# Performance work log

Hardware: AMD Instinct MI355X
Metric: run time of the kernel (lower is better)

The kernel has to match this reference:

```python
import jax, jax.numpy as jnp
import numpy as np
import math

ALPHA = 2.0  # spikingjelly surrogate.ATan default alpha
NB_STEPS, NUM_IN, NUM_HID, NUM_OUT = 100, 784, 100, 10
BATCH = 1024
TAU_LIF = 2.0

@jax.custom_vjp
def atan_spike(x):
    # Heaviside forward, ATan surrogate backward
    return (x >= 0.0).astype(x.dtype)

def _atan_fwd(x):
    return atan_spike(x), x

def _atan_bwd(x, g):
    return (g * (ALPHA / 2.0) / (1.0 + (jnp.pi / 2.0 * ALPHA * x) ** 2),)

atan_spike.defvjp(_atan_fwd, _atan_bwd)


def setup_inputs() -> dict:
    key = jax.random.key(0)
    ks = jax.random.split(key, 3)
    x = jax.random.normal(ks[0], (BATCH, NB_STEPS, NUM_IN), jnp.float32)
    tau_syn = 2.0
    # spikingjelly SynapseFilter(learnable=True): w init = -log(tau - 1)
    w_syn1 = jnp.asarray(-math.log(tau_syn - 1.0), jnp.float32)
    w_syn2 = jnp.asarray(-math.log(tau_syn - 1.0), jnp.float32)
    W1 = jax.random.normal(ks[1], (NUM_HID, NUM_IN), jnp.float32) / np.sqrt(NUM_IN).astype(np.float32)
    b1 = jnp.zeros((NUM_HID,), jnp.float32)
    W2 = jax.random.normal(ks[2], (NUM_OUT, NUM_HID), jnp.float32) / np.sqrt(NUM_HID).astype(np.float32)
    b2 = jnp.zeros((NUM_OUT,), jnp.float32)
    return dict(x=x, w_syn1=w_syn1, W1=W1, b1=b1, w_syn2=w_syn2, W2=W2, b2=b2)


def reference(x, w_syn1, W1, b1, w_syn2, W2, b2):
    B = x.shape[0]
    inv1 = jax.nn.sigmoid(w_syn1)  # 1/tau of filter 1
    inv2 = jax.nn.sigmoid(w_syn2)
    s1 = jnp.zeros((B, NUM_IN), x.dtype)
    v1 = jnp.zeros((B, NUM_HID), x.dtype)
    s2 = jnp.zeros((B, NUM_HID), x.dtype)
    v2 = jnp.zeros((B, NUM_OUT), x.dtype)

    def step(carry, xt):
        s1, v1, s2, v2 = carry
        # SynapseFilter 1: s = s - s*sigmoid(w) + in
        s1 = s1 - s1 * inv1 + xt
        h1 = s1 @ W1.T + b1
        # LIF 1: decay_input=True, v_reset=0: v += (x - (v - 0)) / tau
        v1 = v1 + (h1 - v1) / TAU_LIF
        sp1 = atan_spike(v1 - 1.0)       # v_threshold = 1.0
        v1 = v1 * (1.0 - sp1)            # hard reset to v_reset = 0
        # SynapseFilter 2
        s2 = s2 - s2 * inv2 + sp1
        h2 = s2 @ W2.T + b2
        # LIF 2: v_reset=None (soft reset), v_threshold=0, decay_input=True
        v2 = v2 + (h2 - v2) / TAU_LIF
        sp2 = atan_spike(v2 - 0.0)
        v2 = v2 - sp2 * 0.0              # soft reset subtracts spike*threshold (=0)
        return (s1, v1, s2, v2), None

    (s1, v1, s2, v2), _ = jax.lax.scan(step, (s1, v1, s2, v2), jnp.swapaxes(x, 0, 1))
    # Net.forward returns self.fc[-1].v: final membrane potential of last LIF
    return v2
```

## Files before the change

### kernel.cpp

```cpp
#include <hip/hip_runtime.h>
#include <math.h>


#define NSTEPS 100
#define NHID 100
#define KDIM 784
#define BK 16
#define NOUT 10

__global__ __launch_bounds__(256, 4)
void snn_fused(const float* __restrict__ X, const float* __restrict__ wsyn1p,
               const float* __restrict__ W1, const float* __restrict__ b1,
               const float* __restrict__ wsyn2p, const float* __restrict__ W2,
               const float* __restrict__ b2, float* __restrict__ out) {
  __shared__ float Xs[BK][130];
  __shared__ float Ws[BK][104];
  __shared__ float Cs[25][104];
  __shared__ float zsh[NHID];

  const int tid = threadIdx.x;
  const int l   = tid & 63;
  const int wu  = __builtin_amdgcn_readfirstlane(tid >> 6);
  const int cbase = 28 * wu;
  const long b  = blockIdx.x;
  const float* __restrict__ Xb = X + b * (NSTEPS * KDIM);

  float acc0[28], acc1[28];
#pragma unroll
  for (int c = 0; c < 28; ++c) { acc0[c] = 0.f; acc1[c] = 0.f; }

  const int sr  = tid >> 2;
  const int skq = tid & 3;

  for (int kt = 0; kt < KDIM; kt += BK) {
    const float4 va = *(const float4*)(Xb + sr * KDIM + kt + 4 * skq);
    const int t1 = (sr + 64 < NSTEPS) ? (sr + 64) : (NSTEPS - 1);
    const float4 vb = *(const float4*)(Xb + t1 * KDIM + kt + 4 * skq);
    {
      float2 p0 = {va.x, vb.x}, p1 = {va.y, vb.y};
      float2 p2 = {va.z, vb.z}, p3 = {va.w, vb.w};
      *(float2*)&Xs[4 * skq + 0][2 * sr] = p0;
      *(float2*)&Xs[4 * skq + 1][2 * sr] = p1;
      *(float2*)&Xs[4 * skq + 2][2 * sr] = p2;
      *(float2*)&Xs[4 * skq + 3][2 * sr] = p3;
    }
    for (int i = tid; i < 4 * NHID; i += 256) {
      const int j = i >> 2, kq = i & 3;
      const float4 v = *(const float4*)(W1 + (size_t)j * KDIM + kt + 4 * kq);
      Ws[4 * kq + 0][j] = v.x;
      Ws[4 * kq + 1][j] = v.y;
      Ws[4 * kq + 2][j] = v.z;
      Ws[4 * kq + 3][j] = v.w;
    }
    __syncthreads();

#pragma unroll
    for (int k = 0; k < BK; ++k) {
      const float2 xp = *(const float2*)&Xs[k][2 * l];
#pragma unroll
      for (int c4 = 0; c4 < 7; ++c4) {
        const float4 wv = *(const float4*)&Ws[k][cbase + 4 * c4];
        acc0[4*c4+0] = fmaf(xp.x, wv.x, acc0[4*c4+0]);
        acc0[4*c4+1] = fmaf(xp.x, wv.y, acc0[4*c4+1]);
        acc0[4*c4+2] = fmaf(xp.x, wv.z, acc0[4*c4+2]);
        acc0[4*c4+3] = fmaf(xp.x, wv.w, acc0[4*c4+3]);
        acc1[4*c4+0] = fmaf(xp.y, wv.x, acc1[4*c4+0]);
        acc1[4*c4+1] = fmaf(xp.y, wv.y, acc1[4*c4+1]);
        acc1[4*c4+2] = fmaf(xp.y, wv.z, acc1[4*c4+2]);
        acc1[4*c4+3] = fmaf(xp.y, wv.w, acc1[4*c4+3]);
      }
    }
    __syncthreads();
  }

  const float inv1 = 1.f / (1.f + expf(-wsyn1p[0]));
  const float inv2 = 1.f / (1.f + expf(-wsyn2p[0]));
  const float bj = (tid < NHID) ? b1[tid] : 0.f;
  const int ncols = (cbase + 28 <= NHID) ? 28 : (NHID - cbase);
  float S = 0.f, v1 = 0.f, s2 = 0.f, z = 0.f;
  float at = 0x1p-100f;

  for (int q = 0; q < 4; ++q) {
    const int r0 = l - 25 * q;
    const int r1 = l + 64 - 25 * q;
    if (r0 >= 0 && r0 < 25) {
      for (int c = 0; c < ncols; ++c) Cs[r0][cbase + c] = acc0[c];
    }
    if (r1 >= 0 && r1 < 25) {
      for (int c = 0; c < ncols; ++c) Cs[r1][cbase + c] = acc1[c];
    }
    __syncthreads();
    if (tid < NHID) {
#pragma unroll
      for (int tt = 0; tt < 25; ++tt) {
        const float u = Cs[tt][tid];
        S = S - S * inv1 + u;
        const float h = S + bj;
        v1 = v1 + (h - v1) * 0.5f;
        const float sp = (v1 >= 1.0f) ? 1.0f : 0.0f;
        v1 = v1 * (1.0f - sp);
        s2 = s2 - s2 * inv2 + sp;
        z  = fmaf(at, s2, z);
        at *= 2.0f;
      }
    }
    __syncthreads();
  }

  if (tid < NHID) zsh[tid] = z;
  __syncthreads();

  if (tid < NOUT) {
    float a = b2[tid];
    const float* __restrict__ wrow = W2 + tid * NHID;
#pragma unroll
    for (int jj = 0; jj < NHID; ++jj) a = fmaf(zsh[jj], wrow[jj], a);
    out[b * NOUT + tid] = a;
  }
}

extern "C" void kernel_launch(void* const* d_in, const int* in_sizes, int n_in,
                              void* d_out, int out_size, void* d_ws, size_t ws_size,
                              hipStream_t stream) {
  const float* x     = (const float*)d_in[0];
  const float* wsyn1 = (const float*)d_in[1];
  const float* W1    = (const float*)d_in[2];
  const float* b1    = (const float*)d_in[3];
  const float* wsyn2 = (const float*)d_in[4];
  const float* W2    = (const float*)d_in[5];
  const float* b2    = (const float*)d_in[6];
  float* out = (float*)d_out;

  snn_fused<<<dim3(1024), dim3(256), 0, stream>>>(x, wsyn1, W1, b1, wsyn2, W2,
                                                  b2, out);
}
```

Baseline: 642.3 us.

## Process two batch rows per block with 4x25 register tiles and prefetching

Each block now handles two batch elements (512 blocks), giving each thread a 4-row by 25-column accumulator tile so every W1 tile loaded into shared memory is reused across twice as many rows. It also adds register prefetch of the next X/W1 tile to overlap global loads with FMAs, and removes one barrier per k-step. This cuts redundant W1 traffic and raises FMA-to-LDS-load ratio, at the cost of more registers (launch bounds lowered to 2 blocks/SM) and fewer blocks for latency hiding.

Result: faster. 561.7 us (-12.5%).

```diff
diff --git a/kernel.cpp b/kernel.cpp
--- a/kernel.cpp
+++ b/kernel.cpp
@@ -8,92 +8,126 @@
 #define BK 16
 #define NOUT 10
 
-__global__ __launch_bounds__(256, 4)
-void snn_fused(const float* __restrict__ X, const float* __restrict__ wsyn1p,
-               const float* __restrict__ W1, const float* __restrict__ b1,
-               const float* __restrict__ wsyn2p, const float* __restrict__ W2,
-               const float* __restrict__ b2, float* __restrict__ out) {
-  __shared__ float Xs[BK][130];
-  __shared__ float Ws[BK][104];
-  __shared__ float Cs[25][104];
-  __shared__ float zsh[NHID];
+__global__ __launch_bounds__(256, 2)
+void snn_fused2(const float* __restrict__ X, const float* __restrict__ wsyn1p,
+                const float* __restrict__ W1, const float* __restrict__ b1,
+                const float* __restrict__ wsyn2p, const float* __restrict__ W2,
+                const float* __restrict__ b2, float* __restrict__ out) {
+  __shared__ float Xs[BK][256];
+  __shared__ float Ws[BK][112];
+  __shared__ float Cs[2][25][106];
+  __shared__ float zsh[2][NHID];
 
   const int tid = threadIdx.x;
   const int l   = tid & 63;
-  const int wu  = __builtin_amdgcn_readfirstlane(tid >> 6);
-  const int cbase = 28 * wu;
-  const long b  = blockIdx.x;
-  const float* __restrict__ Xb = X + b * (NSTEPS * KDIM);
+  const int cg  = __builtin_amdgcn_readfirstlane(tid >> 6);
+  const long b0 = 2L * blockIdx.x;
 
-  float acc0[28], acc1[28];
+  const int sb = tid >> 7;
+  const int st = ((tid & 127) < NSTEPS) ? (tid & 127) : (NSTEPS - 1);
+  const float* __restrict__ Xrow = X + ((b0 + sb) * NSTEPS + st) * (size_t)KDIM;
+  const int wj0 = tid >> 2, wkq = tid & 3;
+  const int g0 = wj0 / 25, c0 = wj0 % 25;
+  const int wj1 = wj0 + 64;
+  const int g1 = wj1 / 25, c1 = wj1 % 25;
+  const float* __restrict__ Wp0 = W1 + (size_t)wj0 * KDIM + 4 * wkq;
+  const float* __restrict__ Wp1 = W1 + (size_t)wj1 * KDIM + 4 * wkq;
+
+  float acc[4][25];
 #pragma unroll
-  for (int c = 0; c < 28; ++c) { acc0[c] = 0.f; acc1[c] = 0.f; }
+  for (int i = 0; i < 4; ++i)
+#pragma unroll
+    for (int c = 0; c < 25; ++c) acc[i][c] = 0.0f;
 
-  const int sr  = tid >> 2;
-  const int skq = tid & 3;
+  float4 xr0 = *(const float4*)(Xrow + 0);
+  float4 xr1 = *(const float4*)(Xrow + 4);
+  float4 xr2 = *(const float4*)(Xrow + 8);
+  float4 xr3 = *(const float4*)(Xrow + 12);
+  float4 wr0 = *(const float4*)(Wp0);
+  float4 wr1 = (tid < 144) ? *(const float4*)(Wp1) : float4{0, 0, 0, 0};
 
   for (int kt = 0; kt < KDIM; kt += BK) {
-    const float4 va = *(const float4*)(Xb + sr * KDIM + kt + 4 * skq);
-    const int t1 = (sr + 64 < NSTEPS) ? (sr + 64) : (NSTEPS - 1);
-    const float4 vb = *(const float4*)(Xb + t1 * KDIM + kt + 4 * skq);
+    __syncthreads();
+    Xs[0][tid] = xr0.x;  Xs[1][tid] = xr0.y;  Xs[2][tid] = xr0.z;  Xs[3][tid] = xr0.w;
+    Xs[4][tid] = xr1.x;  Xs[5][tid] = xr1.y;  Xs[6][tid] = xr1.z;  Xs[7][tid] = xr1.w;
+    Xs[8][tid] = xr2.x;  Xs[9][tid] = xr2.y;  Xs[10][tid] = xr2.z; Xs[11][tid] = xr2.w;
+    Xs[12][tid] = xr3.x; Xs[13][tid] = xr3.y; Xs[14][tid] = xr3.z; Xs[15][tid] = xr3.w;
     {
-      float2 p0 = {va.x, vb.x}, p1 = {va.y, vb.y};
-      float2 p2 = {va.z, vb.z}, p3 = {va.w, vb.w};
-      *(float2*)&Xs[4 * skq + 0][2 * sr] = p0;
-      *(float2*)&Xs[4 * skq + 1][2 * sr] = p1;
-      *(float2*)&Xs[4 * skq + 2][2 * sr] = p2;
-      *(float2*)&Xs[4 * skq + 3][2 * sr] = p3;
+      float* w = &Ws[4 * wkq][28 * g0 + c0];
+      w[0] = wr0.x; w[112] = wr0.y; w[224] = wr0.z; w[336] = wr0.w;
     }
-    for (int i = tid; i < 4 * NHID; i += 256) {
-      const int j = i >> 2, kq = i & 3;
-      const float4 v = *(const float4*)(W1 + (size_t)j * KDIM + kt + 4 * kq);
-      Ws[4 * kq + 0][j] = v.x;
-      Ws[4 * kq + 1][j] = v.y;
-      Ws[4 * kq + 2][j] = v.z;
-      Ws[4 * kq + 3][j] = v.w;
+    if (tid < 144) {
+      float* w = &Ws[4 * wkq][28 * g1 + c1];
+      w[0] = wr1.x; w[112] = wr1.y; w[224] = wr1.z; w[336] = wr1.w;
     }
     __syncthreads();
-
+    if (kt + BK < KDIM) {
+      const float* xp = Xrow + kt + BK;
+      xr0 = *(const float4*)(xp + 0);
+      xr1 = *(const float4*)(xp + 4);
+      xr2 = *(const float4*)(xp + 8);
+      xr3 = *(const float4*)(xp + 12);
+      wr0 = *(const float4*)(Wp0 + kt + BK);
+      if (tid < 144) wr1 = *(const float4*)(Wp1 + kt + BK);
+    }
 #pragma unroll
     for (int k = 0; k < BK; ++k) {
-      const float2 xp = *(const float2*)&Xs[k][2 * l];
+      const float4 xv = *(const float4*)&Xs[k][4 * l];
+      const float* __restrict__ wk = &Ws[k][28 * cg];
 #pragma unroll
-      for (int c4 = 0; c4 < 7; ++c4) {
-        const float4 wv = *(const float4*)&Ws[k][cbase + 4 * c4];
-        acc0[4*c4+0] = fmaf(xp.x, wv.x, acc0[4*c4+0]);
-        acc0[4*c4+1] = fmaf(xp.x, wv.y, acc0[4*c4+1]);
-        acc0[4*c4+2] = fmaf(xp.x, wv.z, acc0[4*c4+2]);
-        acc0[4*c4+3] = fmaf(xp.x, wv.w, acc0[4*c4+3]);
-        acc1[4*c4+0] = fmaf(xp.y, wv.x, acc1[4*c4+0]);
-        acc1[4*c4+1] = fmaf(xp.y, wv.y, acc1[4*c4+1]);
-        acc1[4*c4+2] = fmaf(xp.y, wv.z, acc1[4*c4+2]);
-        acc1[4*c4+3] = fmaf(xp.y, wv.w, acc1[4*c4+3]);
+      for (int g = 0; g < 6; ++g) {
+        const float4 wv = *(const float4*)(wk + 4 * g);
+        acc[0][4*g+0] = fmaf(xv.x, wv.x, acc[0][4*g+0]);
+        acc[1][4*g+0] = fmaf(xv.y, wv.x, acc[1][4*g+0]);
+        acc[2][4*g+0] = fmaf(xv.z, wv.x, acc[2][4*g+0]);
+        acc[3][4*g+0] = fmaf(xv.w, wv.x, acc[3][4*g+0]);
+        acc[0][4*g+1] = fmaf(xv.x, wv.y, acc[0][4*g+1]);
+        acc[1][4*g+1] = fmaf(xv.y, wv.y, acc[1][4*g+1]);
+        acc[2][4*g+1] = fmaf(xv.z, wv.y, acc[2][4*g+1]);
+        acc[3][4*g+1] = fmaf(xv.w, wv.y, acc[3][4*g+1]);
+        acc[0][4*g+2] = fmaf(xv.x, wv.z, acc[0][4*g+2]);
+        acc[1][4*g+2] = fmaf(xv.y, wv.z, acc[1][4*g+2]);
+        acc[2][4*g+2] = fmaf(xv.z, wv.z, acc[2][4*g+2]);
+        acc[3][4*g+2] = fmaf(xv.w, wv.z, acc[3][4*g+2]);
+        acc[0][4*g+3] = fmaf(xv.x, wv.w, acc[0][4*g+3]);
+        acc[1][4*g+3] = fmaf(xv.y, wv.w, acc[1][4*g+3]);
+        acc[2][4*g+3] = fmaf(xv.z, wv.w, acc[2][4*g+3]);
+        acc[3][4*g+3] = fmaf(xv.w, wv.w, acc[3][4*g+3]);
       }
+      const float w24 = wk[24];
+      acc[0][24] = fmaf(xv.x, w24, acc[0][24]);
+      acc[1][24] = fmaf(xv.y, w24, acc[1][24]);
+      acc[2][24] = fmaf(xv.z, w24, acc[2][24]);
+      acc[3][24] = fmaf(xv.w, w24, acc[3][24]);
     }
-    __syncthreads();
   }
 
   const float inv1 = 1.f / (1.f + expf(-wsyn1p[0]));
   const float inv2 = 1.f / (1.f + expf(-wsyn2p[0]));
-  const float bj = (tid < NHID) ? b1[tid] : 0.f;
-  const int ncols = (cbase + 28 <= NHID) ? 28 : (NHID - cbase);
+  const int sb2 = tid >> 7;
+  const int j   = tid & 127;
+  const float bj = (j < NHID) ? b1[j] : 0.f;
   float S = 0.f, v1 = 0.f, s2 = 0.f, z = 0.f;
   float at = 0x1p-100f;
 
   for (int q = 0; q < 4; ++q) {
-    const int r0 = l - 25 * q;
-    const int r1 = l + 64 - 25 * q;
-    if (r0 >= 0 && r0 < 25) {
-      for (int c = 0; c < ncols; ++c) Cs[r0][cbase + c] = acc0[c];
-    }
-    if (r1 >= 0 && r1 < 25) {
-      for (int c = 0; c < ncols; ++c) Cs[r1][cbase + c] = acc1[c];
+    __syncthreads();
+#pragma unroll
+    for (int i = 0; i < 4; ++i) {
+      const int r = 4 * l + i;
+      const int bb = r >> 7;
+      const int t  = r & 127;
+      const int tt = t - 25 * q;
+      if (t < NSTEPS && tt >= 0 && tt < 25) {
+#pragma unroll
+        for (int c = 0; c < 25; ++c) Cs[bb][tt][25 * cg + c] = acc[i][c];
+      }
     }
     __syncthreads();
-    if (tid < NHID) {
+    if (j < NHID) {
 #pragma unroll
       for (int tt = 0; tt < 25; ++tt) {
-        const float u = Cs[tt][tid];
+        const float u = Cs[sb2][tt][j];
         S = S - S * inv1 + u;
         const float h = S + bj;
         v1 = v1 + (h - v1) * 0.5f;
@@ -104,18 +138,19 @@
         at *= 2.0f;
       }
     }
-    __syncthreads();
   }
 
-  if (tid < NHID) zsh[tid] = z;
+  if (j < NHID) zsh[sb2][j] = z;
   __syncthreads();
 
-  if (tid < NOUT) {
-    float a = b2[tid];
-    const float* __restrict__ wrow = W2 + tid * NHID;
+  if (tid < 2 * NOUT) {
+    const int bb = tid / NOUT;
+    const int jo = tid % NOUT;
+    float a = b2[jo];
+    const float* __restrict__ wrow = W2 + jo * NHID;
 #pragma unroll
-    for (int jj = 0; jj < NHID; ++jj) a = fmaf(zsh[jj], wrow[jj], a);
-    out[b * NOUT + tid] = a;
+    for (int jj = 0; jj < NHID; ++jj) a = fmaf(zsh[bb][jj], wrow[jj], a);
+    out[(b0 + bb) * NOUT + jo] = a;
   }
 }
 
@@ -131,6 +166,6 @@
   const float* b2    = (const float*)d_in[6];
   float* out = (float*)d_out;
 
-  snn_fused<<<dim3(1024), dim3(256), 0, stream>>>(x, wsyn1, W1, b1, wsyn2, W2,
+  snn_fused2<<<dim3(512), dim3(256), 0, stream>>>(x, wsyn1, W1, b1, wsyn2, W2,
                                                   b2, out);
 }
```
